# Kernel tuning notes

Hardware: AMD Instinct MI355X
Metric: run time of the kernel (lower is better)

## Reference

```python
import jax, jax.numpy as jnp
import numpy as np

B, QL, ML = 8, 128, 1024
QS, KS, H = 512, 512, 256


def setup_inputs() -> dict:
    key = jax.random.key(0)
    ks = jax.random.split(key, 10)
    query = jax.random.normal(ks[0], (B, QL, QS), dtype=jnp.float32)
    memory = jax.random.normal(ks[1], (B, ML, KS), dtype=jnp.float32)
    mask = jax.random.bernoulli(ks[2], 0.1, (B, ML))
    mask = mask.at[:, 0].set(False)  # ensure at least one valid position per row
    s_q = 1.0 / np.sqrt(QS)
    s_k = 1.0 / np.sqrt(KS)
    s_h = 1.0 / np.sqrt(H)
    Wq = jax.random.uniform(ks[3], (H, QS), jnp.float32, -s_q, s_q)
    bq = jax.random.uniform(ks[4], (H,), jnp.float32, -s_q, s_q)
    Wk = jax.random.uniform(ks[5], (H, KS), jnp.float32, -s_k, s_k)
    bk = jax.random.uniform(ks[6], (H,), jnp.float32, -s_k, s_k)
    wl = jax.random.uniform(ks[7], (H,), jnp.float32, -s_h, s_h)
    bl = jax.random.uniform(ks[8], (), jnp.float32, -s_h, s_h)
    return {"query": query, "memory": memory, "mask": mask,
            "Wq": Wq, "bq": bq, "Wk": Wk, "bk": bk, "wl": wl, "bl": bl}


def reference(query, memory, mask, Wq, bq, Wk, bk, wl, bl):
    # q: [B, QL, H], k: [B, ML, H]
    q = jnp.einsum('bqs,hs->bqh', query, Wq) + bq
    k = jnp.einsum('bms,hs->bmh', memory, Wk) + bk
    # additive score: tanh(q + k) projected to scalar  -> [B, QL, ML]
    z = jnp.tanh(q[:, :, None, :] + k[:, None, :, :])  # [B, QL, ML, H]
    logits = jnp.einsum('bqmh,h->bqm', z, wl) + bl
    logits = jnp.where(mask[:, None, :], jnp.float32(-1e18), logits)
    weights = jax.nn.softmax(logits, axis=-1)  # BottleSoftmax over mem_len
    attns = jnp.einsum('bqm,bms->bqs', weights, memory)
    return attns, weights
```

## Files before the change

kernel.cpp:

```cpp
#include <hip/hip_runtime.h>

#define B_  8
#define QL_ 128
#define ML_ 1024
#define KS_ 512
#define H_  256

#define QP_OFF 0
#define KP_OFF 262144
#define MASK_OFF 2359296
#define WH_OFF 2361344
#define WL_OFF 2492416
#define MT_H_OFF 2623488
#define MT_L_OFF 4720640
#define WB_H_OFF 6817792
#define WB_L_OFF 7342080
#define XH_OFF 7866368
#define XL_OFF 10225664
#define WLP_OFF 12584960

typedef __attribute__((ext_vector_type(8))) short bfrag;
typedef __attribute__((ext_vector_type(4))) float f4acc;
typedef __attribute__((ext_vector_type(2))) float f2;

__device__ __forceinline__ void split1(float v, unsigned& h, unsigned& lo) {
    unsigned u  = __float_as_uint(v);
    unsigned hb = u & 0xFFFF0000u;
    float    lf = v - __uint_as_float(hb);
    unsigned ul = __float_as_uint(lf);
    unsigned lr = ul + 0x7FFFu + ((ul >> 16) & 1u);
    h  = u >> 16;
    lo = lr >> 16;
}

__device__ __forceinline__ void split4(const float4& a, unsigned& h01, unsigned& h23,
                                       unsigned& l01, unsigned& l23) {
    unsigned h[4], l[4];
    split1(a.x, h[0], l[0]); split1(a.y, h[1], l[1]);
    split1(a.z, h[2], l[2]); split1(a.w, h[3], l[3]);
    h01 = h[0] | (h[1] << 16); h23 = h[2] | (h[3] << 16);
    l01 = l[0] | (l[1] << 16); l23 = l[2] | (l[3] << 16);
}

__global__ __launch_bounds__(256) void prep_kernel(
    const float* __restrict__ query, const float* __restrict__ memory,
    const float* __restrict__ Wq, const float* __restrict__ Wk,
    const float* __restrict__ wl,
    unsigned short* __restrict__ Whi, unsigned short* __restrict__ Wlo,
    unsigned short* __restrict__ Xhi, unsigned short* __restrict__ Xlo,
    const unsigned char* __restrict__ mraw, unsigned char* __restrict__ mout,
    float* __restrict__ wlp) {
    const int bid = blockIdx.x;
    const int t = threadIdx.x;

    if (bid == 1216) {
        wlp[(t & ~7) | (((t & 3) << 1) | ((t >> 2) & 1))] = wl[t];
        __shared__ int s_not01, s_not0f;
        const unsigned int* w = (const unsigned int*)mraw;
        if (t == 0) { s_not01 = 0; s_not0f = 0; }
        __syncthreads();
        int not01 = 0, not0f = 0;
        for (int i = t; i < 2048; i += 256) {
            unsigned int v = w[i];
            if (v != 0u && v != 1u) not01 = 1;
            if (v != 0u && v != 0x3F800000u) not0f = 1;
        }
        if (not01) atomicOr(&s_not01, 1);
        if (not0f) atomicOr(&s_not0f, 1);
        __syncthreads();
        int wordTyped = (!s_not01) || (!s_not0f);
        for (int i = t; i < B_ * ML_; i += 256) {
            unsigned char mv;
            if (wordTyped) mv = (w[i] != 0u) ? 1 : 0;
            else           mv = mraw[i] ? 1 : 0;
            mout[i] = mv;
        }
        return;
    }

    const float* src; unsigned short *dh, *dl; size_t soff, doff;
    if (bid < 64) {
        src = (bid < 32) ? Wq : Wk;
        soff = (size_t)(bid & 31) * 4096;
        doff = ((bid < 32) ? 0 : 131072) + soff;
        dh = Whi; dl = Wlo;
    } else if (bid < 192) {
        src = query;  soff = (size_t)(bid - 64) * 4096;  doff = soff;
        dh = Xhi; dl = Xlo;
    } else {
        src = memory; soff = (size_t)(bid - 192) * 4096; doff = 524288 + soff;
        dh = Xhi; dl = Xlo;
    }
    soff += (size_t)t * 16; doff += (size_t)t * 16;

    unsigned hw[8], lw[8];
#pragma unroll
    for (int i = 0; i < 4; ++i) {
        float4 v = *(const float4*)(src + soff + i * 4);
        split4(v, hw[i * 2], hw[i * 2 + 1], lw[i * 2], lw[i * 2 + 1]);
    }
    *(uint4*)(dh + doff)     = make_uint4(hw[0], hw[1], hw[2], hw[3]);
    *(uint4*)(dh + doff + 8) = make_uint4(hw[4], hw[5], hw[6], hw[7]);
    *(uint4*)(dl + doff)     = make_uint4(lw[0], lw[1], lw[2], lw[3]);
    *(uint4*)(dl + doff + 8) = make_uint4(lw[4], lw[5], lw[6], lw[7]);
}

__global__ __launch_bounds__(256) void proj_kernel(
    const unsigned short* __restrict__ Xhi, const unsigned short* __restrict__ Xlo,
    const unsigned short* __restrict__ Whi, const unsigned short* __restrict__ Wlo,
    const float* __restrict__ bq, const float* __restrict__ bk,
    float* __restrict__ Eq, float* __restrict__ Ek) {
    const int bid = blockIdx.x;
    const int t = threadIdx.x;
    const int wk = (bid & 7) * 144 + (bid >> 3);
    const int nt = wk & 3;
    const int mt = wk >> 2;

    const bool isQ = (mt < 32);
    const int arow0 = mt * 32;
    const int orow0 = isQ ? arow0 : arow0 - 1024;
    const float* bias = isQ ? bq : bk;
    float* out = isQ ? Eq : Ek;
    const int wrb = (isQ ? 0 : 256) + nt * 64;

    const int w  = t >> 6;
    const int wm = w >> 1, wn = w & 1;
    const int l  = t & 63;
    const int lr = l & 15, lk = l >> 4;

    __shared__ unsigned short As[2][2][32][64];
    __shared__ unsigned short Bs[2][2][64][64];

    const int pa   = t >> 7;
    const int slot = t & 127;
    const int arow = slot >> 2, ao = slot & 3;
    const int brow = slot >> 1, bo0 = (slot & 1) * 4;
    const unsigned short* asrc = (pa ? Xlo : Xhi) + (size_t)(arow0 + arow) * 512 + ao * 8;
    const unsigned short* bsrc = (pa ? Wlo : Whi) + (size_t)(wrb + brow) * 512 + bo0 * 8;
    const int awd0 = (ao ^ (arow & 7)) * 8;
    const int awd1 = ((ao + 4) ^ (arow & 7)) * 8;
    int bwd[4];
#pragma unroll
    for (int i = 0; i < 4; ++i) bwd[i] = ((bo0 + i) ^ (brow & 7)) * 8;

    f4acc acc[2];
    acc[0] = (f4acc){0.f, 0.f, 0.f, 0.f};
    acc[1] = (f4acc){0.f, 0.f, 0.f, 0.f};

    uint4 g0a0, g0a1, g0b0, g0b1, g0b2, g0b3;
    uint4 g1a0, g1a1, g1b0, g1b1, g1b2, g1b3;

#define LOADG(G, c) do {                                                  \
    G##a0 = *(const uint4*)(asrc + (size_t)(c) * 64);                     \
    G##a1 = *(const uint4*)(asrc + (size_t)(c) * 64 + 32);                \
    G##b0 = *(const uint4*)(bsrc + (size_t)(c) * 64);                     \
    G##b1 = *(const uint4*)(bsrc + (size_t)(c) * 64 + 8);                 \
    G##b2 = *(const uint4*)(bsrc + (size_t)(c) * 64 + 16);                \
    G##b3 = *(const uint4*)(bsrc + (size_t)(c) * 64 + 24); } while (0)

#define WRITEB(P, G) do {                                                 \
    *(uint4*)(&As[P][pa][arow][awd0])  = G##a0;                           \
    *(uint4*)(&As[P][pa][arow][awd1])  = G##a1;                           \
    *(uint4*)(&Bs[P][pa][brow][bwd[0]]) = G##b0;                          \
    *(uint4*)(&Bs[P][pa][brow][bwd[1]]) = G##b1;                          \
    *(uint4*)(&Bs[P][pa][brow][bwd[2]]) = G##b2;                          \
    *(uint4*)(&Bs[P][pa][brow][bwd[3]]) = G##b3; } while (0)

#define COMPUTE(P) do {                                                   \
    _Pragma("unroll")                                                     \
    for (int ks = 0; ks < 2; ++ks) {                                      \
        const int ra = wm * 16 + lr;                                      \
        const int koA = ((ks * 4 + lk) ^ (ra & 7)) * 8;                   \
        bfrag ah = *(const bfrag*)&As[P][0][ra][koA];                     \
        bfrag al = *(const bfrag*)&As[P][1][ra][koA];                     \
        _Pragma("unroll")                                                 \
        for (int ni = 0; ni < 2; ++ni) {                                  \
            const int rb = wn * 32 + ni * 16 + lr;                        \
            const int koB = ((ks * 4 + lk) ^ (rb & 7)) * 8;               \
            bfrag bh = *(const bfrag*)&Bs[P][0][rb][koB];                 \
            bfrag bl = *(const bfrag*)&Bs[P][1][rb][koB];                 \
            acc[ni] = __builtin_amdgcn_mfma_f32_16x16x32_bf16(            \
                ah, bh, acc[ni], 0, 0, 0);                                \
            acc[ni] = __builtin_amdgcn_mfma_f32_16x16x32_bf16(            \
                ah, bl, acc[ni], 0, 0, 0);                                \
            acc[ni] = __builtin_amdgcn_mfma_f32_16x16x32_bf16(            \
                al, bh, acc[ni], 0, 0, 0);                                \
        }                                                                 \
    } } while (0)

    LOADG(g0, 0);
    WRITEB(0, g0);
    LOADG(g1, 1);
    __syncthreads();

#pragma unroll
    for (int c = 0; c < 8; ++c) {
        if (c + 1 < 8) {
            if ((c + 1) & 1) WRITEB(1, g1); else WRITEB(0, g0);
        }
        if (c + 2 < 8) {
            if (c & 1) LOADG(g1, c + 2); else LOADG(g0, c + 2);
        }
        COMPUTE(c & 1);
        __syncthreads();
    }
#undef LOADG
#undef WRITEB
#undef COMPUTE

    const float SC = 2.885390081777926815f;
#pragma unroll
    for (int ni = 0; ni < 2; ++ni) {
        const int col = nt * 64 + wn * 32 + ni * 16 + lr;
        const int colp = (col & ~7) | (((col & 3) << 1) | ((col >> 2) & 1));
        const float bc = bias[col];
#pragma unroll
        for (int rr = 0; rr < 4; ++rr) {
            const int row = orow0 + wm * 16 + lk * 4 + rr;
            out[(size_t)row * 256 + colp] =
                __builtin_amdgcn_exp2f(SC * (acc[ni][rr] + bc));
        }
    }
}

__device__ __forceinline__ f2 qterm8(const float4 k4a, const float4 k4b,
                                     const float4 q4a, const float4 q4b,
                                     const float4 w4a, const float4 w4b,
                                     f2 acc) {
    f2 kp0 = {k4a.x, k4a.y}, kp1 = {k4a.z, k4a.w};
    f2 kp2 = {k4b.x, k4b.y}, kp3 = {k4b.z, k4b.w};
    f2 qp0 = {q4a.x, q4a.y}, qp1 = {q4a.z, q4a.w};
    f2 qp2 = {q4b.x, q4b.y}, qp3 = {q4b.z, q4b.w};
    f2 wp0 = {w4a.x, w4a.y}, wp1 = {w4a.z, w4a.w};
    f2 wp2 = {w4b.x, w4b.y}, wp3 = {w4b.z, w4b.w};
    const f2 one2 = {1.0f, 1.0f};
    f2 pp0 = __builtin_elementwise_fma(kp0, qp0, one2);
    f2 pp1 = __builtin_elementwise_fma(kp1, qp1, one2);
    f2 pp2 = __builtin_elementwise_fma(kp2, qp2, one2);
    f2 pp3 = __builtin_elementwise_fma(kp3, qp3, one2);
    f2 p01 = pp0 * pp1, p23 = pp2 * pp3;
    f2 n01 = __builtin_elementwise_fma(wp1, pp0, wp0 * pp1);
    f2 n23 = __builtin_elementwise_fma(wp3, pp2, wp2 * pp3);
    f2 Nm  = __builtin_elementwise_fma(n23, p01, n01 * p23);
    f2 P   = p01 * p23;
    f2 r   = {__builtin_amdgcn_rcpf(P.x), __builtin_amdgcn_rcpf(P.y)};
    return __builtin_elementwise_fma(Nm, r, acc);
}

__global__ __launch_bounds__(256) void logits_kernel(
    const float* __restrict__ Eq, const float* __restrict__ Ek,
    const float* __restrict__ wlp, float* __restrict__ sr) {
    const int bid = blockIdx.x;
    const int b  = bid & 7;
    const int r2 = bid >> 3;
    const int mt = r2 & 15;
    const int qt = r2 >> 4;
    const int tid = threadIdx.x;
    const int m  = tid & 63;
    const int qh = __builtin_amdgcn_readfirstlane(tid >> 6);

    __shared__ float kq[2][8][64][4];

    const float* q0 = Eq + ((size_t)(b * QL_ + qt * 8 + qh * 2)) * H_;
    const float* q1 = q0 + H_;
    const float* kpb = Ek + ((size_t)(b * ML_ + mt * 64)) * H_;

    const int srow = tid & 63;
    const int sq   = tid >> 6;
    const float* kst = kpb + (size_t)srow * H_ + 8 * sq;

    float4 a0 = *(const float4*)(kst);
    float4 a1 = *(const float4*)(kst + 4);
    *(float4*)(&kq[0][2 * sq + 0][srow][0]) = a0;
    *(float4*)(&kq[0][2 * sq + 1][srow][0]) = a1;
    a0 = *(const float4*)(kst + 32);
    a1 = *(const float4*)(kst + 36);
    __syncthreads();

    f2 accp[2];
    accp[0] = (f2){0.f, 0.f};
    accp[1] = (f2){0.f, 0.f};

    for (int c = 0; c < 8; ++c) {
        const int cb = c & 1;
        if (c < 7) {
            *(float4*)(&kq[cb ^ 1][2 * sq + 0][srow][0]) = a0;
            *(float4*)(&kq[cb ^ 1][2 * sq + 1][srow][0]) = a1;
            if (c < 6) {
                a0 = *(const float4*)(kst + (c + 2) * 32);
                a1 = *(const float4*)(kst + (c + 2) * 32 + 4);
            }
        }
        const int h0 = c * 32;
#pragma unroll
        for (int pg = 0; pg < 4; ++pg) {
            float4 k4a = *(const float4*)(&kq[cb][2 * pg + 0][m][0]);
            float4 k4b = *(const float4*)(&kq[cb][2 * pg + 1][m][0]);
            float4 w4a = *(const float4*)(wlp + h0 + pg * 8);
            float4 w4b = *(const float4*)(wlp + h0 + pg * 8 + 4);
            float4 q4a = *(const float4*)(q0 + h0 + pg * 8);
            float4 q4b = *(const float4*)(q0 + h0 + pg * 8 + 4);
            accp[0] = qterm8(k4a, k4b, q4a, q4b, w4a, w4b, accp[0]);
            q4a = *(const float4*)(q1 + h0 + pg * 8);
            q4b = *(const float4*)(q1 + h0 + pg * 8 + 4);
            accp[1] = qterm8(k4a, k4b, q4a, q4b, w4a, w4b, accp[1]);
        }
        __syncthreads();
    }
    const size_t ro = ((size_t)(b * QL_ + qt * 8 + qh * 2)) * ML_ + mt * 64 + m;
    sr[ro]       = accp[0].x + accp[0].y;
    sr[ro + ML_] = accp[1].x + accp[1].y;
}

__global__ __launch_bounds__(256) void softmax_kernel(
    float* __restrict__ wrow_io, const unsigned char* __restrict__ mv,
    unsigned short* __restrict__ Wbhi, unsigned short* __restrict__ Wblo,
    const float* __restrict__ memory,
    unsigned short* __restrict__ MThi, unsigned short* __restrict__ MTlo) {
    const int tid = threadIdx.x;

    if (blockIdx.x >= 1024) {
        const int idx = blockIdx.x - 1024;
        const int b  = idx >> 7;
        const int r  = idx & 127;
        const int mt = r >> 3;
        const int st = r & 7;
        __shared__ float T[64][68];

        const int i  = tid >> 2, jb = (tid & 3) << 4;
        const float* mp = memory + ((size_t)(b * ML_ + mt * 64 + i)) * KS_ + st * 64 + jb;
#pragma unroll
        for (int q = 0; q < 4; ++q)
            *(float4*)(&T[i][jb + q * 4]) = *(const float4*)(mp + q * 4);
        __syncthreads();

        const int s = tid >> 2, mb = (tid & 3) << 4;
        unsigned hh[16], ll[16];
#pragma unroll
        for (int e = 0; e < 16; ++e) split1(T[mb + e][s], hh[e], ll[e]);
        unsigned hp[8], lp[8];
#pragma unroll
        for (int e = 0; e < 8; ++e) {
            hp[e] = hh[2 * e] | (hh[2 * e + 1] << 16);
            lp[e] = ll[2 * e] | (ll[2 * e + 1] << 16);
        }
        const size_t doff = ((size_t)(b * KS_ + st * 64 + s)) * ML_ + mt * 64 + mb;
        *(uint4*)(MThi + doff)     = make_uint4(hp[0], hp[1], hp[2], hp[3]);
        *(uint4*)(MThi + doff + 8) = make_uint4(hp[4], hp[5], hp[6], hp[7]);
        *(uint4*)(MTlo + doff)     = make_uint4(lp[0], lp[1], lp[2], lp[3]);
        *(uint4*)(MTlo + doff + 8) = make_uint4(lp[4], lp[5], lp[6], lp[7]);
        return;
    }

    const int row = blockIdx.x;
    const int b = row >> 7;
    float* srow = wrow_io + (size_t)row * ML_;
    const unsigned char* mrow = mv + b * ML_;
    __shared__ float red[4];

    float4 s4 = *(const float4*)(srow + tid * 4);
    uchar4 m4 = *(const uchar4*)(mrow + tid * 4);
    float l[4];
    l[0] = m4.x ? -1e18f : -2.0f * s4.x;
    l[1] = m4.y ? -1e18f : -2.0f * s4.y;
    l[2] = m4.z ? -1e18f : -2.0f * s4.z;
    l[3] = m4.w ? -1e18f : -2.0f * s4.w;

    float mx = fmaxf(fmaxf(l[0], l[1]), fmaxf(l[2], l[3]));
#pragma unroll
    for (int off = 32; off >= 1; off >>= 1)
        mx = fmaxf(mx, __shfl_xor(mx, off));
    if ((tid & 63) == 0) red[tid >> 6] = mx;
    __syncthreads();
    mx = fmaxf(fmaxf(red[0], red[1]), fmaxf(red[2], red[3]));
    __syncthreads();

    const float L2E = 1.44269504088896340736f;
    float e[4], s = 0.f;
#pragma unroll
    for (int i = 0; i < 4; ++i) {
        e[i] = __builtin_amdgcn_exp2f((l[i] - mx) * L2E);
        s += e[i];
    }
#pragma unroll
    for (int off = 32; off >= 1; off >>= 1)
        s += __shfl_xor(s, off);
    if ((tid & 63) == 0) red[tid >> 6] = s;
    __syncthreads();
    s = (red[0] + red[1]) + (red[2] + red[3]);
    float inv = __builtin_amdgcn_rcpf(s);
    float4 o = make_float4(e[0] * inv, e[1] * inv, e[2] * inv, e[3] * inv);
    *(float4*)(srow + tid * 4) = o;

    unsigned h01, h23, l01, l23;
    split4(o, h01, h23, l01, l23);
    *(uint2*)(Wbhi + (size_t)row * ML_ + tid * 4) = make_uint2(h01, h23);
    *(uint2*)(Wblo + (size_t)row * ML_ + tid * 4) = make_uint2(l01, l23);
}

__global__ __launch_bounds__(256) void attn_out_kernel(
    const unsigned short* __restrict__ Wbhi, const unsigned short* __restrict__ Wblo,
    const unsigned short* __restrict__ MThi, const unsigned short* __restrict__ MTlo,
    float* __restrict__ out) {
    const int bid = blockIdx.x;
    const int b  = bid & 7;
    const int r  = bid >> 3;
    const int mt = r & 7;
    const int nt = r >> 3;
    const int t = threadIdx.x;
    const int w  = t >> 6;
    const int l  = t & 63;
    const int lr = l & 15, lk = l >> 4;

    __shared__ unsigned short As[2][16][2][64];
    __shared__ unsigned short Bs[2][64][2][64];

    const int pa  = t >> 7;
    const int ar  = (t >> 3) & 15;
    const int acq = t & 7;
    const unsigned short* asrc = (pa ? Wblo : Wbhi)
        + ((size_t)(b * QL_ + mt * 16 + ar)) * ML_ + acq * 8;
    const int aws = (acq ^ (ar & 7)) * 8;

    const int pb  = t >> 7;
    const int br  = (t & 127) >> 1;
    const int bq0 = (t & 1) * 4;
    const unsigned short* bsrc = (pb ? MTlo : MThi)
        + ((size_t)(b * KS_ + nt * 64 + br)) * ML_ + bq0 * 8;
    int bws[4];
#pragma unroll
    for (int i2 = 0; i2 < 4; ++i2) bws[i2] = ((bq0 + i2) ^ (br & 7)) * 8;

    f4acc acc = (f4acc){0.f, 0.f, 0.f, 0.f};

    uint4 g0a, g0b0, g0b1, g0b2, g0b3;
    uint4 g1a, g1b0, g1b1, g1b2, g1b3;

#define LOADG(G, c) do {                                                  \
    G##a  = *(const uint4*)(asrc + (size_t)(c) * 64);                     \
    G##b0 = *(const uint4*)(bsrc + (size_t)(c) * 64);                     \
    G##b1 = *(const uint4*)(bsrc + (size_t)(c) * 64 + 8);                 \
    G##b2 = *(const uint4*)(bsrc + (size_t)(c) * 64 + 16);                \
    G##b3 = *(const uint4*)(bsrc + (size_t)(c) * 64 + 24); } while (0)

#define WRITEB(P, G) do {                                                 \
    *(uint4*)(&As[P][ar][pa][aws])    = G##a;                             \
    *(uint4*)(&Bs[P][br][pb][bws[0]]) = G##b0;                            \
    *(uint4*)(&Bs[P][br][pb][bws[1]]) = G##b1;                            \
    *(uint4*)(&Bs[P][br][pb][bws[2]]) = G##b2;                            \
    *(uint4*)(&Bs[P][br][pb][bws[3]]) = G##b3; } while (0)

#define COMPUTE(P) do {                                                   \
    _Pragma("unroll")                                                     \
    for (int ks = 0; ks < 2; ++ks) {                                      \
        const int k8 = (ks * 4 + lk) ^ (lr & 7);                          \
        bfrag ah = *(const bfrag*)&As[P][lr][0][k8 * 8];                  \
        bfrag al = *(const bfrag*)&As[P][lr][1][k8 * 8];                  \
        bfrag bh = *(const bfrag*)&Bs[P][w * 16 + lr][0][k8 * 8];         \
        bfrag bl = *(const bfrag*)&Bs[P][w * 16 + lr][1][k8 * 8];         \
        acc = __builtin_amdgcn_mfma_f32_16x16x32_bf16(ah, bh, acc, 0,0,0);\
        acc = __builtin_amdgcn_mfma_f32_16x16x32_bf16(ah, bl, acc, 0,0,0);\
        acc = __builtin_amdgcn_mfma_f32_16x16x32_bf16(al, bh, acc, 0,0,0);\
    } } while (0)

    LOADG(g0, 0);
    WRITEB(0, g0);
    LOADG(g1, 1);
    __syncthreads();

#pragma unroll
    for (int c = 0; c < 16; ++c) {
        if (c + 1 < 16) {
            if ((c + 1) & 1) WRITEB(1, g1); else WRITEB(0, g0);
        }
        if (c + 2 < 16) {
            if (c & 1) LOADG(g1, c + 2); else LOADG(g0, c + 2);
        }
        COMPUTE(c & 1);
        __syncthreads();
    }
#undef LOADG
#undef WRITEB
#undef COMPUTE

    const int col = nt * 64 + w * 16 + lr;
#pragma unroll
    for (int rr = 0; rr < 4; ++rr) {
        const int row = mt * 16 + lk * 4 + rr;
        out[((size_t)(b * QL_ + row)) * KS_ + col] = acc[rr];
    }
}

extern "C" void kernel_launch(void* const* d_in, const int* in_sizes, int n_in,
                              void* d_out, int out_size, void* d_ws, size_t ws_size,
                              hipStream_t stream) {
    const float* query  = (const float*)d_in[0];
    const float* memory = (const float*)d_in[1];
    const unsigned char* mask = (const unsigned char*)d_in[2];
    const float* Wq = (const float*)d_in[3];
    const float* bq = (const float*)d_in[4];
    const float* Wk = (const float*)d_in[5];
    const float* bk = (const float*)d_in[6];
    const float* wl = (const float*)d_in[7];

    float* ws = (float*)d_ws;
    float* Eq = ws + QP_OFF;
    float* Ek = ws + KP_OFF;
    unsigned char* mcan = (unsigned char*)(ws + MASK_OFF);
    unsigned short* Whi  = (unsigned short*)(ws + WH_OFF);
    unsigned short* Wlo  = (unsigned short*)(ws + WL_OFF);
    unsigned short* MThi = (unsigned short*)(ws + MT_H_OFF);
    unsigned short* MTlo = (unsigned short*)(ws + MT_L_OFF);
    unsigned short* Wbhi = (unsigned short*)(ws + WB_H_OFF);
    unsigned short* Wblo = (unsigned short*)(ws + WB_L_OFF);
    unsigned short* Xhi  = (unsigned short*)(ws + XH_OFF);
    unsigned short* Xlo  = (unsigned short*)(ws + XL_OFF);
    float* wlp = ws + WLP_OFF;

    float* attns = (float*)d_out;
    float* wout  = (float*)d_out + B_ * QL_ * KS_;

    prep_kernel<<<dim3(1217), dim3(256), 0, stream>>>(query, memory, Wq, Wk, wl,
                                                      Whi, Wlo, Xhi, Xlo, mask, mcan, wlp);
    proj_kernel<<<dim3(1152), dim3(256), 0, stream>>>(Xhi, Xlo, Whi, Wlo,
                                                      bq, bk, Eq, Ek);
    logits_kernel<<<dim3(2048), dim3(256), 0, stream>>>(Eq, Ek, wlp, wout);
    softmax_kernel<<<dim3(2048), dim3(256), 0, stream>>>(wout, mcan, Wbhi, Wblo,
                                                         memory, MThi, MTlo);
    attn_out_kernel<<<dim3(512), dim3(256), 0, stream>>>(Wbhi, Wblo, MThi, MTlo, attns);
}
```

Baseline: 158.5 us.

## Move memory transpose-split into prep kernel and double logits query rows per thread

The bf16 hi/lo transpose of memory moves from the softmax kernel into the prep kernel, which gains 1024 extra blocks. The softmax kernel now only does the row softmax. The logits kernel computes 4 query rows per thread instead of 2, halving its grid and reusing each staged key tile across more queries. This lowers LDS traffic per logit but raises register pressure and leaves fewer blocks to fill the GPU.

Measured after the change: 161.1 us. Within noise of the previous version (+1.6%).

```diff
diff --git a/kernel.cpp b/kernel.cpp
--- a/kernel.cpp
+++ b/kernel.cpp
@@ -48,12 +48,13 @@
     const float* __restrict__ wl,
     unsigned short* __restrict__ Whi, unsigned short* __restrict__ Wlo,
     unsigned short* __restrict__ Xhi, unsigned short* __restrict__ Xlo,
+    unsigned short* __restrict__ MThi, unsigned short* __restrict__ MTlo,
     const unsigned char* __restrict__ mraw, unsigned char* __restrict__ mout,
     float* __restrict__ wlp) {
     const int bid = blockIdx.x;
     const int t = threadIdx.x;
 
-    if (bid == 1216) {
+    if (bid == 2240) {
         wlp[(t & ~7) | (((t & 3) << 1) | ((t >> 2) & 1))] = wl[t];
         __shared__ int s_not01, s_not0f;
         const unsigned int* w = (const unsigned int*)mraw;
@@ -75,6 +76,39 @@
             else           mv = mraw[i] ? 1 : 0;
             mout[i] = mv;
         }
+        return;
+    }
+
+    if (bid >= 1216) {
+        const int idx = bid - 1216;
+        const int b  = idx >> 7;
+        const int r  = idx & 127;
+        const int mt = r >> 3;
+        const int st = r & 7;
+        __shared__ float T[64][68];
+
+        const int i  = t >> 2, jb = (t & 3) << 4;
+        const float* mp = memory + ((size_t)(b * ML_ + mt * 64 + i)) * KS_ + st * 64 + jb;
+#pragma unroll
+        for (int q = 0; q < 4; ++q)
+            *(float4*)(&T[i][jb + q * 4]) = *(const float4*)(mp + q * 4);
+        __syncthreads();
+
+        const int s = t >> 2, mb = (t & 3) << 4;
+        unsigned hh[16], ll[16];
+#pragma unroll
+        for (int e = 0; e < 16; ++e) split1(T[mb + e][s], hh[e], ll[e]);
+        unsigned hp[8], lp[8];
+#pragma unroll
+        for (int e = 0; e < 8; ++e) {
+            hp[e] = hh[2 * e] | (hh[2 * e + 1] << 16);
+            lp[e] = ll[2 * e] | (ll[2 * e + 1] << 16);
+        }
+        const size_t doff = ((size_t)(b * KS_ + st * 64 + s)) * ML_ + mt * 64 + mb;
+        *(uint4*)(MThi + doff)     = make_uint4(hp[0], hp[1], hp[2], hp[3]);
+        *(uint4*)(MThi + doff + 8) = make_uint4(hp[4], hp[5], hp[6], hp[7]);
+        *(uint4*)(MTlo + doff)     = make_uint4(lp[0], lp[1], lp[2], lp[3]);
+        *(uint4*)(MTlo + doff + 8) = make_uint4(lp[4], lp[5], lp[6], lp[7]);
         return;
     }
 
@@ -261,8 +295,7 @@
 
     __shared__ float kq[2][8][64][4];
 
-    const float* q0 = Eq + ((size_t)(b * QL_ + qt * 8 + qh * 2)) * H_;
-    const float* q1 = q0 + H_;
+    const float* q0 = Eq + ((size_t)(b * QL_ + qt * 16 + qh * 4)) * H_;
     const float* kpb = Ek + ((size_t)(b * ML_ + mt * 64)) * H_;
 
     const int srow = tid & 63;
@@ -277,9 +310,9 @@
     a1 = *(const float4*)(kst + 36);
     __syncthreads();
 
-    f2 accp[2];
-    accp[0] = (f2){0.f, 0.f};
-    accp[1] = (f2){0.f, 0.f};
+    f2 accp[4];
+#pragma unroll
+    for (int j = 0; j < 4; ++j) accp[j] = (f2){0.f, 0.f};
 
     for (int c = 0; c < 8; ++c) {
         const int cb = c & 1;
@@ -298,62 +331,27 @@
             float4 k4b = *(const float4*)(&kq[cb][2 * pg + 1][m][0]);
             float4 w4a = *(const float4*)(wlp + h0 + pg * 8);
             float4 w4b = *(const float4*)(wlp + h0 + pg * 8 + 4);
-            float4 q4a = *(const float4*)(q0 + h0 + pg * 8);
-            float4 q4b = *(const float4*)(q0 + h0 + pg * 8 + 4);
-            accp[0] = qterm8(k4a, k4b, q4a, q4b, w4a, w4b, accp[0]);
-            q4a = *(const float4*)(q1 + h0 + pg * 8);
-            q4b = *(const float4*)(q1 + h0 + pg * 8 + 4);
-            accp[1] = qterm8(k4a, k4b, q4a, q4b, w4a, w4b, accp[1]);
+#pragma unroll
+            for (int j = 0; j < 4; ++j) {
+                float4 q4a = *(const float4*)(q0 + (size_t)j * H_ + h0 + pg * 8);
+                float4 q4b = *(const float4*)(q0 + (size_t)j * H_ + h0 + pg * 8 + 4);
+                accp[j] = qterm8(k4a, k4b, q4a, q4b, w4a, w4b, accp[j]);
+            }
         }
         __syncthreads();
     }
-    const size_t ro = ((size_t)(b * QL_ + qt * 8 + qh * 2)) * ML_ + mt * 64 + m;
-    sr[ro]       = accp[0].x + accp[0].y;
-    sr[ro + ML_] = accp[1].x + accp[1].y;
+    const size_t ro = ((size_t)(b * QL_ + qt * 16 + qh * 4)) * ML_ + mt * 64 + m;
+#pragma unroll
+    for (int j = 0; j < 4; ++j)
+        sr[ro + (size_t)j * ML_] = accp[j].x + accp[j].y;
 }
 
 __global__ __launch_bounds__(256) void softmax_kernel(
     float* __restrict__ wrow_io, const unsigned char* __restrict__ mv,
-    unsigned short* __restrict__ Wbhi, unsigned short* __restrict__ Wblo,
-    const float* __restrict__ memory,
-    unsigned short* __restrict__ MThi, unsigned short* __restrict__ MTlo) {
-    const int tid = threadIdx.x;
-
-    if (blockIdx.x >= 1024) {
-        const int idx = blockIdx.x - 1024;
-        const int b  = idx >> 7;
-        const int r  = idx & 127;
-        const int mt = r >> 3;
-        const int st = r & 7;
-        __shared__ float T[64][68];
-
-        const int i  = tid >> 2, jb = (tid & 3) << 4;
-        const float* mp = memory + ((size_t)(b * ML_ + mt * 64 + i)) * KS_ + st * 64 + jb;
-#pragma unroll
-        for (int q = 0; q < 4; ++q)
-            *(float4*)(&T[i][jb + q * 4]) = *(const float4*)(mp + q * 4);
-        __syncthreads();
-
-        const int s = tid >> 2, mb = (tid & 3) << 4;
-        unsigned hh[16], ll[16];
-#pragma unroll
-        for (int e = 0; e < 16; ++e) split1(T[mb + e][s], hh[e], ll[e]);
-        unsigned hp[8], lp[8];
-#pragma unroll
-        for (int e = 0; e < 8; ++e) {
-            hp[e] = hh[2 * e] | (hh[2 * e + 1] << 16);
-            lp[e] = ll[2 * e] | (ll[2 * e + 1] << 16);
-        }
-        const size_t doff = ((size_t)(b * KS_ + st * 64 + s)) * ML_ + mt * 64 + mb;
-        *(uint4*)(MThi + doff)     = make_uint4(hp[0], hp[1], hp[2], hp[3]);
-        *(uint4*)(MThi + doff + 8) = make_uint4(hp[4], hp[5], hp[6], hp[7]);
-        *(uint4*)(MTlo + doff)     = make_uint4(lp[0], lp[1], lp[2], lp[3]);
-        *(uint4*)(MTlo + doff + 8) = make_uint4(lp[4], lp[5], lp[6], lp[7]);
-        return;
-    }
-
+    unsigned short* __restrict__ Wbhi, unsigned short* __restrict__ Wblo) {
     const int row = blockIdx.x;
     const int b = row >> 7;
+    const int tid = threadIdx.x;
     float* srow = wrow_io + (size_t)row * ML_;
     const unsigned char* mrow = mv + b * ML_;
     __shared__ float red[4];
@@ -520,12 +518,12 @@
     float* attns = (float*)d_out;
     float* wout  = (float*)d_out + B_ * QL_ * KS_;
 
-    prep_kernel<<<dim3(1217), dim3(256), 0, stream>>>(query, memory, Wq, Wk, wl,
-                                                      Whi, Wlo, Xhi, Xlo, mask, mcan, wlp);
+    prep_kernel<<<dim3(2241), dim3(256), 0, stream>>>(query, memory, Wq, Wk, wl,
+                                                      Whi, Wlo, Xhi, Xlo,
+                                                      MThi, MTlo, mask, mcan, wlp);
     proj_kernel<<<dim3(1152), dim3(256), 0, stream>>>(Xhi, Xlo, Whi, Wlo,
                                                       bq, bk, Eq, Ek);
-    logits_kernel<<<dim3(2048), dim3(256), 0, stream>>>(Eq, Ek, wlp, wout);
-    softmax_kernel<<<dim3(2048), dim3(256), 0, stream>>>(wout, mcan, Wbhi, Wblo,
-                                                         memory, MThi, MTlo);
+    logits_kernel<<<dim3(1024), dim3(256), 0, stream>>>(Eq, Ek, wlp, wout);
+    softmax_kernel<<<dim3(B_ * QL_), dim3(256), 0, stream>>>(wout, mcan, Wbhi, Wblo);
     attn_out_kernel<<<dim3(512), dim3(256), 0, stream>>>(Wbhi, Wblo, MThi, MTlo, attns);
 }
```
